# Kernel tuning notes

Hardware: AMD Instinct MI355X
Metric: run time of the kernel (lower is better)

## Reference

```python
import jax, jax.numpy as jnp
import numpy as np

B, N, K = 4096, 87, 87


def setup_inputs() -> dict:
    key = jax.random.key(0)
    ks = jax.random.split(key, 6)
    x = jax.random.normal(ks[0], (B, N, N), dtype=jnp.float32)
    evals = jax.random.uniform(ks[1], (B, K), dtype=jnp.float32)
    evecs = jax.random.normal(ks[2], (B, N, K), dtype=jnp.float32)
    # learned per-node diffusion times (torch inits to 0, clamped to 1e-8;
    # use small positive values to exercise the exp decay)
    diffusion_time = jax.random.uniform(ks[3], (N,), dtype=jnp.float32) * 0.1
    # MiniMLP: single Linear(2*N -> N)
    lim = 1.0 / np.sqrt(2 * N)
    W = jax.random.uniform(ks[4], (N, 2 * N), minval=-lim, maxval=lim, dtype=jnp.float32)
    b = jax.random.uniform(ks[5], (N,), minval=-lim, maxval=lim, dtype=jnp.float32)
    return {"x": x, "evals": evals, "evecs": evecs,
            "diffusion_time": diffusion_time, "W": W, "b": b}


def reference(x, evals, evecs, diffusion_time, W, b):
    # clamp diffusion times (torch does this in-place on .data)
    t = jnp.maximum(diffusion_time, 1e-8)                     # (N,)
    # expa[b,i,m] = exp(-t_i * eval[b,m])
    expa = jnp.exp(-t[None, :, None] * evals[:, None, :])     # (B,N,K)
    # kernel[b,i,j] = sum_m evec[b,i,m] * expa[b,i,m] * evec[b,j,m]
    # (equivalent to the diag_embed + triple matmul + diagonal in the torch code)
    kernel = jnp.einsum('bim,bjm->bij', evecs * expa, evecs)  # (B,N,N)
    x_diffuse = jnp.concatenate([x, kernel], axis=2)          # (B,N,2N)
    return x_diffuse @ W.T + b                                # (B,N,N)
```

## Files before the change

### kernel.cpp

```cpp
#include <hip/hip_runtime.h>
#include <hip/hip_bf16.h>
#include <math.h>

#define NN    87
#define NN2   (NN * NN)
#define SPH   104
#define RP    96
#define PANEL (RP * SPH)
#define NT    256

#define WS_NEED (2 * PANEL * 2)

typedef __attribute__((ext_vector_type(8))) short bf16x8;
typedef __attribute__((ext_vector_type(4))) short bf16x4;
typedef __attribute__((ext_vector_type(4))) float f32x4;
typedef float f32x4u __attribute__((ext_vector_type(4), aligned(4)));

__device__ __forceinline__ short f2bf(float f) {
    __hip_bfloat16 h = __float2bfloat16(f);
    return *(short*)&h;
}
__device__ __forceinline__ float bf2f(short s) {
    union { unsigned u; float f; } v;
    v.u = ((unsigned)(unsigned short)s) << 16;
    return v.f;
}

__global__ void prep(const float* __restrict__ W, short* __restrict__ wp) {
    int idx = (int)blockIdx.x * NT + (int)threadIdx.x;
    if (idx >= 2 * PANEL) return;
    int p = idx / PANEL, rem = idx - p * PANEL;
    int r = rem / SPH, c = rem - r * SPH;
    short v = 0;
    if (r < NN && c < NN) v = f2bf(W[r * (2 * NN) + p * NN + c]);
    wp[idx] = v;
}

template <bool WS>
__device__ __forceinline__ bf16x8 wload(const short* __restrict__ wp,
                                        const float* __restrict__ gW,
                                        int panel, int jrow, int jcl, int k0, bool tailKs)
{
    if constexpr (WS) {
        return *(const bf16x8*)&wp[panel * PANEL + jrow * SPH + k0];
    } else {
        float v[8];
        if (!tailKs) {
            f32x4u a  = *(const f32x4u*)(gW + jcl * (2 * NN) + panel * NN + k0);
            f32x4u b4 = *(const f32x4u*)(gW + jcl * (2 * NN) + panel * NN + k0 + 4);
            v[0] = a.x; v[1] = a.y; v[2] = a.z; v[3] = a.w;
            v[4] = b4.x; v[5] = b4.y; v[6] = b4.z; v[7] = b4.w;
        } else {
            #pragma unroll
            for (int q = 0; q < 8; ++q) {
                int k = k0 + q;
                v[q] = (k < NN) ? gW[jcl * (2 * NN) + panel * NN + k] : 0.f;
            }
        }
        bf16x8 o;
        #pragma unroll
        for (int q = 0; q < 8; ++q) o[q] = f2bf(v[q]);
        return o;
    }
}

template <bool WS>
__global__ __launch_bounds__(NT, 4)
void fused(const float* __restrict__ gx, const float* __restrict__ gevals,
           const float* __restrict__ gevecs, const float* __restrict__ dtime,
           const float* __restrict__ gW, const float* __restrict__ bias,
           const short* __restrict__ wp, float* __restrict__ out)
{
    __shared__ __align__(16) char smem[2 * PANEL * 2];
    short* const sE = (short*)smem;
    short* const sX = (short*)(smem + PANEL * 2);
    short* const sD = (short*)smem;
    float* const sF = (float*)smem;
    __shared__ float sLam[RP];

    const int b    = (int)blockIdx.x;
    const int tid  = (int)threadIdx.x;
    const int lane = tid & 63;
    const int wave = tid >> 6;
    const int l15  = lane & 15;
    const int lk   = lane >> 4;
    const int i0   = (wave >> 1) * 48;
    const int j0   = (wave & 1) * 48;

    const float* __restrict__ Eb   = gevecs + (size_t)b * NN2;
    const float* __restrict__ xb   = gx     + (size_t)b * NN2;
    const float* __restrict__ lamb = gevals + (size_t)b * NN;

    if (tid < RP) sLam[tid] = (tid < NN) ? lamb[tid] : 0.f;

    for (int u = tid; u < NN * 22; u += NT) {
        int r = u / 22, sg = u - r * 22, c = sg * 4;
        const float* pE = Eb + r * NN + c;
        const float* pX = xb + r * NN + c;
        float e0, e1, e2, e3, x0, x1, x2, x3;
        if (sg < 21) {
            f32x4u te = *(const f32x4u*)pE; e0 = te.x; e1 = te.y; e2 = te.z; e3 = te.w;
            f32x4u tx = *(const f32x4u*)pX; x0 = tx.x; x1 = tx.y; x2 = tx.z; x3 = tx.w;
        } else {
            e0 = pE[0]; e1 = pE[1]; e2 = pE[2]; e3 = 0.f;
            x0 = pX[0]; x1 = pX[1]; x2 = pX[2]; x3 = 0.f;
        }
        bf16x4 we = {f2bf(e0), f2bf(e1), f2bf(e2), f2bf(e3)};
        bf16x4 wx = {f2bf(x0), f2bf(x1), f2bf(x2), f2bf(x3)};
        *(bf16x4*)&sE[r * SPH + c] = we;
        *(bf16x4*)&sX[r * SPH + c] = wx;
    }
    {
        const bf16x4 z = {0, 0, 0, 0};
        for (int u = tid; u < 9 * 26; u += NT) {
            int r = NN + u / 26, c = (u % 26) * 4;
            *(bf16x4*)&sE[r * SPH + c] = z;
            *(bf16x4*)&sX[r * SPH + c] = z;
        }
        for (int u = tid; u < NN * 4; u += NT) {
            int r = u >> 2, c = 88 + (u & 3) * 4;
            *(bf16x4*)&sE[r * SPH + c] = z;
            *(bf16x4*)&sX[r * SPH + c] = z;
        }
    }
    __syncthreads();

    int ir[3], jr[3];
    float tr_[3];
    #pragma unroll
    for (int r = 0; r < 3; ++r) {
        ir[r] = i0 + 16 * r + l15;
        jr[r] = j0 + 16 * r + l15;
        tr_[r] = fmaxf(dtime[ir[r] < NN ? ir[r] : NN - 1], 1e-8f);
    }

    f32x4 acc1[3][3];
    #pragma unroll
    for (int c = 0; c < 3; ++c)
        #pragma unroll
        for (int r = 0; r < 3; ++r) acc1[c][r] = (f32x4){0.f, 0.f, 0.f, 0.f};

    #pragma unroll
    for (int ks = 0; ks < 3; ++ks) {
        const int k0 = ks * 32 + lk * 8;
        f32x4 la  = *(const f32x4*)&sLam[k0];
        f32x4 lb4 = *(const f32x4*)&sLam[k0 + 4];
        float l8_[8] = {la.x, la.y, la.z, la.w, lb4.x, lb4.y, lb4.z, lb4.w};

        bf16x8 ef[3], af[3];
        #pragma unroll
        for (int c = 0; c < 3; ++c) {
            bf16x4 lo = *(const bf16x4*)&sE[jr[c] * SPH + k0];
            bf16x4 hi = *(const bf16x4*)&sE[jr[c] * SPH + k0 + 4];
            #pragma unroll
            for (int q = 0; q < 4; ++q) { ef[c][q] = lo[q]; ef[c][q + 4] = hi[q]; }
        }
        #pragma unroll
        for (int r = 0; r < 3; ++r) {
            bf16x4 lo = *(const bf16x4*)&sE[ir[r] * SPH + k0];
            bf16x4 hi = *(const bf16x4*)&sE[ir[r] * SPH + k0 + 4];
            #pragma unroll
            for (int q = 0; q < 4; ++q) {
                af[r][q]     = f2bf(bf2f(lo[q]) * __expf(-tr_[r] * l8_[q]));
                af[r][q + 4] = f2bf(bf2f(hi[q]) * __expf(-tr_[r] * l8_[q + 4]));
            }
        }
        #pragma unroll
        for (int c = 0; c < 3; ++c)
            #pragma unroll
            for (int r = 0; r < 3; ++r)
                acc1[c][r] = __builtin_amdgcn_mfma_f32_16x16x32_bf16(ef[c], af[r], acc1[c][r], 0, 0, 0);
    }
    __syncthreads();

    #pragma unroll
    for (int c = 0; c < 3; ++c) {
        const int jb = j0 + 16 * c + lk * 4;
        #pragma unroll
        for (int r = 0; r < 3; ++r) {
            const int i = i0 + 16 * r + l15;
            bf16x4 v = {f2bf(acc1[c][r][0]), f2bf(acc1[c][r][1]),
                        f2bf(acc1[c][r][2]), f2bf(acc1[c][r][3])};
            *(bf16x4*)&sD[i * SPH + jb] = v;
        }
    }
    __builtin_amdgcn_sched_barrier(0);

    f32x4 acc2[3][3];
    #pragma unroll
    for (int wr = 0; wr < 3; ++wr)
        #pragma unroll
        for (int xc = 0; xc < 3; ++xc) acc2[wr][xc] = (f32x4){0.f, 0.f, 0.f, 0.f};

    #pragma unroll
    for (int ks = 0; ks < 3; ++ks) {
        const int k0 = ks * 32 + lk * 8;
        bf16x8 wf[3], xf[3];
        #pragma unroll
        for (int wr = 0; wr < 3; ++wr) {
            int jc = jr[wr] < NN ? jr[wr] : NN - 1;
            wf[wr] = wload<WS>(wp, gW, 0, jr[wr], jc, k0, ks == 2);
        }
        #pragma unroll
        for (int xc = 0; xc < 3; ++xc) {
            bf16x4 lo = *(const bf16x4*)&sX[ir[xc] * SPH + k0];
            bf16x4 hi = *(const bf16x4*)&sX[ir[xc] * SPH + k0 + 4];
            #pragma unroll
            for (int q = 0; q < 4; ++q) { xf[xc][q] = lo[q]; xf[xc][q + 4] = hi[q]; }
        }
        #pragma unroll
        for (int wr = 0; wr < 3; ++wr)
            #pragma unroll
            for (int xc = 0; xc < 3; ++xc)
                acc2[wr][xc] = __builtin_amdgcn_mfma_f32_16x16x32_bf16(wf[wr], xf[xc], acc2[wr][xc], 0, 0, 0);
    }
    __syncthreads();

    #pragma unroll
    for (int ks = 0; ks < 3; ++ks) {
        const int k0 = ks * 32 + lk * 8;
        bf16x8 wf[3], df[3];
        #pragma unroll
        for (int wr = 0; wr < 3; ++wr) {
            int jc = jr[wr] < NN ? jr[wr] : NN - 1;
            wf[wr] = wload<WS>(wp, gW, 1, jr[wr], jc, k0, ks == 2);
        }
        #pragma unroll
        for (int xc = 0; xc < 3; ++xc) {
            bf16x4 lo = *(const bf16x4*)&sD[ir[xc] * SPH + k0];
            bf16x4 hi = *(const bf16x4*)&sD[ir[xc] * SPH + k0 + 4];
            #pragma unroll
            for (int q = 0; q < 4; ++q) { df[xc][q] = lo[q]; df[xc][q + 4] = hi[q]; }
        }
        #pragma unroll
        for (int wr = 0; wr < 3; ++wr)
            #pragma unroll
            for (int xc = 0; xc < 3; ++xc)
                acc2[wr][xc] = __builtin_amdgcn_mfma_f32_16x16x32_bf16(wf[wr], df[xc], acc2[wr][xc], 0, 0, 0);
    }
    __syncthreads();

    #pragma unroll
    for (int wr = 0; wr < 3; ++wr) {
        const int jb = j0 + 16 * wr + lk * 4;
        float bj[4];
        if (jb + 3 < NN) {
            f32x4u t = *(const f32x4u*)(bias + jb);
            bj[0] = t.x; bj[1] = t.y; bj[2] = t.z; bj[3] = t.w;
        } else {
            #pragma unroll
            for (int q = 0; q < 4; ++q) bj[q] = (jb + q < NN) ? bias[jb + q] : 0.f;
        }
        #pragma unroll
        for (int xc = 0; xc < 3; ++xc) {
            const int i = i0 + 16 * xc + l15;
            #pragma unroll
            for (int q = 0; q < 4; ++q) {
                const int j = jb + q;
                if (j < NN) sF[i * NN + j] = acc2[wr][xc][q] + bj[q];
            }
        }
    }
    __syncthreads();

    {
        float* __restrict__ gb = out + (size_t)b * NN2;
        const int s = (4 - ((b * NN2) & 3)) & 3;
        if (tid < s) gb[tid] = sF[tid];
        const int C = (NN2 - s) >> 2;
        for (int m = tid; m < C; m += NT) {
            const int n = s + 4 * m;
            f32x4 v;
            v.x = sF[n]; v.y = sF[n + 1]; v.z = sF[n + 2]; v.w = sF[n + 3];
            *(f32x4*)(gb + n) = v;
        }
        const int tl = s + 4 * C;
        if (tid < NN2 - tl) gb[tl + tid] = sF[tl + tid];
    }
}

extern "C" void kernel_launch(void* const* d_in, const int* in_sizes, int n_in,
                              void* d_out, int out_size, void* d_ws, size_t ws_size,
                              hipStream_t stream)
{
    const float* x     = (const float*)d_in[0];
    const float* evals = (const float*)d_in[1];
    const float* evecs = (const float*)d_in[2];
    const float* dtime = (const float*)d_in[3];
    const float* W     = (const float*)d_in[4];
    const float* bias  = (const float*)d_in[5];
    float* out = (float*)d_out;

    const int B = in_sizes[1] / NN;

    if (ws_size >= (size_t)WS_NEED) {
        short* wp = (short*)d_ws;
        prep<<<(2 * PANEL + NT - 1) / NT, NT, 0, stream>>>(W, wp);
        fused<true><<<dim3(B), dim3(NT), 0, stream>>>(x, evals, evecs, dtime, W, bias, wp, out);
    } else {
        fused<false><<<dim3(B), dim3(NT), 0, stream>>>(x, evals, evecs, dtime, W, bias, nullptr, out);
    }
}
```

Baseline: 103.1 us.

## Swizzle LDS tiles and prefetch W fragments into registers early

```diff
diff --git a/kernel.cpp b/kernel.cpp
--- a/kernel.cpp
+++ b/kernel.cpp
@@ -4,12 +4,13 @@
 
 #define NN    87
 #define NN2   (NN * NN)
-#define SPH   104
 #define RP    96
-#define PANEL (RP * SPH)
+#define SW    128
+#define WPH   104
+#define WPANEL (RP * WPH)
 #define NT    256
 
-#define WS_NEED (2 * PANEL * 2)
+#define WS_NEED (2 * WPANEL * 2)
 
 typedef __attribute__((ext_vector_type(8))) short bf16x8;
 typedef __attribute__((ext_vector_type(4))) short bf16x4;
@@ -26,11 +27,16 @@
     return v.f;
 }
 
+__device__ __forceinline__ int swz(int row, int col) {
+    int m = ((row & 7) << 3) | (((row >> 3) & 1) << 2);
+    return row * SW + (col ^ m);
+}
+
 __global__ void prep(const float* __restrict__ W, short* __restrict__ wp) {
     int idx = (int)blockIdx.x * NT + (int)threadIdx.x;
-    if (idx >= 2 * PANEL) return;
-    int p = idx / PANEL, rem = idx - p * PANEL;
-    int r = rem / SPH, c = rem - r * SPH;
+    if (idx >= 2 * WPANEL) return;
+    int p = idx / WPANEL, rem = idx - p * WPANEL;
+    int r = rem / WPH, c = rem - r * WPH;
     short v = 0;
     if (r < NN && c < NN) v = f2bf(W[r * (2 * NN) + p * NN + c]);
     wp[idx] = v;
@@ -42,7 +48,7 @@
                                         int panel, int jrow, int jcl, int k0, bool tailKs)
 {
     if constexpr (WS) {
-        return *(const bf16x8*)&wp[panel * PANEL + jrow * SPH + k0];
+        return *(const bf16x8*)&wp[panel * WPANEL + jrow * WPH + k0];
     } else {
         float v[8];
         if (!tailKs) {
@@ -65,16 +71,16 @@
 }
 
 template <bool WS>
-__global__ __launch_bounds__(NT, 4)
+__global__ __launch_bounds__(NT, 3)
 void fused(const float* __restrict__ gx, const float* __restrict__ gevals,
            const float* __restrict__ gevecs, const float* __restrict__ dtime,
            const float* __restrict__ gW, const float* __restrict__ bias,
            const short* __restrict__ wp, float* __restrict__ out)
 {
-    __shared__ __align__(16) char smem[2 * PANEL * 2];
-    short* const sE = (short*)smem;
-    short* const sX = (short*)(smem + PANEL * 2);
-    short* const sD = (short*)smem;
+    __shared__ __align__(16) short smem[2 * RP * SW];
+    short* const sE = smem;
+    short* const sX = smem + RP * SW;
+    short* const sD = smem;
     float* const sF = (float*)smem;
     __shared__ float sLam[RP];
 
@@ -92,6 +98,24 @@
     const float* __restrict__ lamb = gevals + (size_t)b * NN;
 
     if (tid < RP) sLam[tid] = (tid < NN) ? lamb[tid] : 0.f;
+
+    int ir[3], jr[3];
+    float tr_[3];
+    #pragma unroll
+    for (int r = 0; r < 3; ++r) {
+        ir[r] = i0 + 16 * r + l15;
+        jr[r] = j0 + 16 * r + l15;
+        tr_[r] = fmaxf(dtime[ir[r] < NN ? ir[r] : NN - 1], 1e-8f);
+    }
+
+    bf16x8 wfx[3][3];
+    #pragma unroll
+    for (int ks = 0; ks < 3; ++ks)
+        #pragma unroll
+        for (int wr = 0; wr < 3; ++wr) {
+            int jc = jr[wr] < NN ? jr[wr] : NN - 1;
+            wfx[ks][wr] = wload<WS>(wp, gW, 0, jr[wr], jc, ks * 32 + lk * 8, ks == 2);
+        }
 
     for (int u = tid; u < NN * 22; u += NT) {
         int r = u / 22, sg = u - r * 22, c = sg * 4;
@@ -107,32 +131,23 @@
         }
         bf16x4 we = {f2bf(e0), f2bf(e1), f2bf(e2), f2bf(e3)};
         bf16x4 wx = {f2bf(x0), f2bf(x1), f2bf(x2), f2bf(x3)};
-        *(bf16x4*)&sE[r * SPH + c] = we;
-        *(bf16x4*)&sX[r * SPH + c] = wx;
+        *(bf16x4*)&sE[swz(r, c)] = we;
+        *(bf16x4*)&sX[swz(r, c)] = wx;
     }
     {
         const bf16x4 z = {0, 0, 0, 0};
-        for (int u = tid; u < 9 * 26; u += NT) {
-            int r = NN + u / 26, c = (u % 26) * 4;
-            *(bf16x4*)&sE[r * SPH + c] = z;
-            *(bf16x4*)&sX[r * SPH + c] = z;
-        }
-        for (int u = tid; u < NN * 4; u += NT) {
-            int r = u >> 2, c = 88 + (u & 3) * 4;
-            *(bf16x4*)&sE[r * SPH + c] = z;
-            *(bf16x4*)&sX[r * SPH + c] = z;
-        }
-    }
-    __syncthreads();
-
-    int ir[3], jr[3];
-    float tr_[3];
-    #pragma unroll
-    for (int r = 0; r < 3; ++r) {
-        ir[r] = i0 + 16 * r + l15;
-        jr[r] = j0 + 16 * r + l15;
-        tr_[r] = fmaxf(dtime[ir[r] < NN ? ir[r] : NN - 1], 1e-8f);
-    }
+        for (int u = tid; u < 9 * 24; u += NT) {
+            int r = NN + u / 24, c = (u % 24) * 4;
+            *(bf16x4*)&sE[swz(r, c)] = z;
+            *(bf16x4*)&sX[swz(r, c)] = z;
+        }
+        for (int u = tid; u < NN * 2; u += NT) {
+            int r = u >> 1, c = 88 + (u & 1) * 4;
+            *(bf16x4*)&sE[swz(r, c)] = z;
+            *(bf16x4*)&sX[swz(r, c)] = z;
+        }
+    }
+    __syncthreads();
 
     f32x4 acc1[3][3];
     #pragma unroll
@@ -150,15 +165,15 @@
         bf16x8 ef[3], af[3];
         #pragma unroll
         for (int c = 0; c < 3; ++c) {
-            bf16x4 lo = *(const bf16x4*)&sE[jr[c] * SPH + k0];
-            bf16x4 hi = *(const bf16x4*)&sE[jr[c] * SPH + k0 + 4];
+            bf16x4 lo = *(const bf16x4*)&sE[swz(jr[c], k0)];
+            bf16x4 hi = *(const bf16x4*)&sE[swz(jr[c], k0 + 4)];
             #pragma unroll
             for (int q = 0; q < 4; ++q) { ef[c][q] = lo[q]; ef[c][q + 4] = hi[q]; }
         }
         #pragma unroll
         for (int r = 0; r < 3; ++r) {
-            bf16x4 lo = *(const bf16x4*)&sE[ir[r] * SPH + k0];
-            bf16x4 hi = *(const bf16x4*)&sE[ir[r] * SPH + k0 + 4];
+            bf16x4 lo = *(const bf16x4*)&sE[swz(ir[r], k0)];
+            bf16x4 hi = *(const bf16x4*)&sE[swz(ir[r], k0 + 4)];
             #pragma unroll
             for (int q = 0; q < 4; ++q) {
                 af[r][q]     = f2bf(bf2f(lo[q]) * __expf(-tr_[r] * l8_[q]));
@@ -173,6 +188,15 @@
     }
     __syncthreads();
 
+    bf16x8 wfd[3][3];
+    #pragma unroll
+    for (int ks = 0; ks < 3; ++ks)
+        #pragma unroll
+        for (int wr = 0; wr < 3; ++wr) {
+            int jc = jr[wr] < NN ? jr[wr] : NN - 1;
+            wfd[ks][wr] = wload<WS>(wp, gW, 1, jr[wr], jc, ks * 32 + lk * 8, ks == 2);
+        }
+
     #pragma unroll
     for (int c = 0; c < 3; ++c) {
         const int jb = j0 + 16 * c + lk * 4;
@@ -181,7 +205,7 @@
             const int i = i0 + 16 * r + l15;
             bf16x4 v = {f2bf(acc1[c][r][0]), f2bf(acc1[c][r][1]),
                         f2bf(acc1[c][r][2]), f2bf(acc1[c][r][3])};
-            *(bf16x4*)&sD[i * SPH + jb] = v;
+            *(bf16x4*)&sD[swz(i, jb)] = v;
         }
     }
     __builtin_amdgcn_sched_barrier(0);
@@ -195,16 +219,11 @@
     #pragma unroll
     for (int ks = 0; ks < 3; ++ks) {
         const int k0 = ks * 32 + lk * 8;
-        bf16x8 wf[3], xf[3];
-        #pragma unroll
-        for (int wr = 0; wr < 3; ++wr) {
-            int jc = jr[wr] < NN ? jr[wr] : NN - 1;
-            wf[wr] = wload<WS>(wp, gW, 0, jr[wr], jc, k0, ks == 2);
-        }
+        bf16x8 xf[3];
         #pragma unroll
         for (int xc = 0; xc < 3; ++xc) {
-            bf16x4 lo = *(const bf16x4*)&sX[ir[xc] * SPH + k0];
-            bf16x4 hi = *(const bf16x4*)&sX[ir[xc] * SPH + k0 + 4];
+            bf16x4 lo = *(const bf16x4*)&sX[swz(ir[xc], k0)];
+            bf16x4 hi = *(const bf16x4*)&sX[swz(ir[xc], k0 + 4)];
             #pragma unroll
             for (int q = 0; q < 4; ++q) { xf[xc][q] = lo[q]; xf[xc][q + 4] = hi[q]; }
         }
@@ -212,23 +231,18 @@
         for (int wr = 0; wr < 3; ++wr)
             #pragma unroll
             for (int xc = 0; xc < 3; ++xc)
-                acc2[wr][xc] = __builtin_amdgcn_mfma_f32_16x16x32_bf16(wf[wr], xf[xc], acc2[wr][xc], 0, 0, 0);
+                acc2[wr][xc] = __builtin_amdgcn_mfma_f32_16x16x32_bf16(wfx[ks][wr], xf[xc], acc2[wr][xc], 0, 0, 0);
     }
     __syncthreads();
 
     #pragma unroll
     for (int ks = 0; ks < 3; ++ks) {
         const int k0 = ks * 32 + lk * 8;
-        bf16x8 wf[3], df[3];
-        #pragma unroll
-        for (int wr = 0; wr < 3; ++wr) {
-            int jc = jr[wr] < NN ? jr[wr] : NN - 1;
-            wf[wr] = wload<WS>(wp, gW, 1, jr[wr], jc, k0, ks == 2);
-        }
+        bf16x8 df[3];
         #pragma unroll
         for (int xc = 0; xc < 3; ++xc) {
-            bf16x4 lo = *(const bf16x4*)&sD[ir[xc] * SPH + k0];
-            bf16x4 hi = *(const bf16x4*)&sD[ir[xc] * SPH + k0 + 4];
+            bf16x4 lo = *(const bf16x4*)&sD[swz(ir[xc], k0)];
+            bf16x4 hi = *(const bf16x4*)&sD[swz(ir[xc], k0 + 4)];
             #pragma unroll
             for (int q = 0; q < 4; ++q) { df[xc][q] = lo[q]; df[xc][q + 4] = hi[q]; }
         }
@@ -236,7 +250,7 @@
         for (int wr = 0; wr < 3; ++wr)
             #pragma unroll
             for (int xc = 0; xc < 3; ++xc)
-                acc2[wr][xc] = __builtin_amdgcn_mfma_f32_16x16x32_bf16(wf[wr], df[xc], acc2[wr][xc], 0, 0, 0);
+                acc2[wr][xc] = __builtin_amdgcn_mfma_f32_16x16x32_bf16(wfd[ks][wr], df[xc], acc2[wr][xc], 0, 0, 0);
     }
     __syncthreads();
 
@@ -295,7 +309,7 @@
 
     if (ws_size >= (size_t)WS_NEED) {
         short* wp = (short*)d_ws;
-        prep<<<(2 * PANEL + NT - 1) / NT, NT, 0, stream>>>(W, wp);
+        prep<<<(2 * WPANEL + NT - 1) / NT, NT, 0, stream>>>(W, wp);
         fused<true><<<dim3(B), dim3(NT), 0, stream>>>(x, evals, evecs, dtime, W, bias, wp, out);
     } else {
         fused<false><<<dim3(B), dim3(NT), 0, stream>>>(x, evals, evecs, dtime, W, bias, nullptr, out);
```

New measurement: 106.1 us. 1.03x slower.
